# Optimization experiments

Hardware: AMD Instinct MI355X
Metric: run time of the kernel (lower is better)

The kernel has to match this reference:

```python
import jax, jax.numpy as jnp
import numpy as np
import math

B, H, N, D = 2, 16, 8192, 64
NUM_PROJS = 7
BLOCK = 256   # key block size
SAMPLE = 256  # number of sampled columns


def _gray_perm(n):
    # AngularLSH._unit_hamming_distance_array: Gray-code ordering of 2**n buckets
    a = np.array([0, 1], dtype=np.int32)
    for i in range(1, n):
        a = np.concatenate([a, a[::-1] + 2 ** i])
    return a

PERM = jnp.asarray(_gray_perm(NUM_PROJS))
ENC = jnp.asarray(2 ** np.arange(NUM_PROJS), dtype=jnp.int32)


def lsh_hash(x, proj_dir):
    # sign-bit angular LSH, then Gray-code remap so nearby buckets share bits
    bits = (jnp.einsum('bhnd,dr->bhnr', x, proj_dir) > 0).astype(jnp.int32)
    bin_ids = (bits * ENC).sum(-1)
    return PERM[bin_ids]


def take_seq(x, idx):
    # gather along the sequence axis (axis=2); idx is [B,H,M]
    return jnp.take_along_axis(x, idx[..., None], axis=2)


def setup_inputs() -> dict:
    key = jax.random.key(0)
    ks = jax.random.split(key, 5)
    return {
        'query': jax.random.normal(ks[0], (B, H, N, D), jnp.float32),
        'key': jax.random.normal(ks[1], (B, H, N, D), jnp.float32),
        'value': jax.random.normal(ks[2], (B, H, N, D), jnp.float32),
        'proj_dir': jax.random.normal(ks[3], (D + 1, NUM_PROJS), jnp.float32),
        'sampled_set': jax.random.randint(ks[4], (B, H, SAMPLE), 0, N),
    }


def reference(query, key, value, proj_dir, sampled_set):
    scale = D ** -0.5

    # asymmetric MIPS transform: key gets sqrt(max||k||^2 - ||k||^2), query gets 0
    k_norm = jnp.linalg.norm(key, axis=-1)                 # [B,H,N]
    k_max = jnp.max(k_norm, axis=-1, keepdims=True)        # [B,H,1]
    k_extra = jnp.sqrt(jnp.maximum(k_max ** 2 - k_norm ** 2, 0.0))
    key_aug = jnp.concatenate([key, k_extra[..., None]], axis=-1)
    query_aug = jnp.concatenate([query, jnp.zeros_like(query[..., :1])], axis=-1)

    # stable sort by LSH bucket; inverse permutation to un-sort queries at the end
    q_idx = jnp.argsort(lsh_hash(query_aug, proj_dir), axis=2, stable=True)
    k_idx = jnp.argsort(lsh_hash(key_aug, proj_dir), axis=2, stable=True)
    q_idx_inv = jnp.argsort(q_idx, axis=2, stable=True)

    q_s = take_seq(query, q_idx)
    k_s = take_seq(key, k_idx)
    v_s = take_seq(value, k_idx)

    nb = N // BLOCK      # number of key blocks (N divisible by BLOCK here)
    qbs = N // nb        # query block size

    # 1) block-diagonal exact attention over LSH-sorted blocks
    qb = q_s.reshape(B, H, nb, qbs, D)
    kb = k_s.reshape(B, H, nb, BLOCK, D)
    vb = v_s.reshape(B, H, nb, BLOCK, D)
    s_blk = jnp.einsum('bhgqd,bhgkd->bhgqk', qb, kb) * scale
    lse_blk = jax.nn.logsumexp(s_blk, axis=-1)             # [B,H,nb,qbs]
    attn_blk = jnp.einsum('bhgqk,bhgkd->bhgqd', jax.nn.softmax(s_blk, axis=-1), vb)
    attn_blk = attn_blk.reshape(B, H, N, D)
    lse_blk = lse_blk.reshape(B, H, N, 1)

    # 2) residual via uniformly sampled columns; mask out columns already in the
    #    query's own diagonal block to avoid double counting
    k_sub = take_seq(k_s, sampled_set)                     # [B,H,S,D]
    v_sub = take_seq(v_s, sampled_set)
    q_blk_id = jnp.arange(N) // qbs                        # [N]
    covered = q_blk_id[None, None, :, None] == (sampled_set // BLOCK)[:, :, None, :]
    bias = jnp.where(covered, jnp.finfo(q_s.dtype).min, 0.0)
    s_res = jnp.einsum('bhnd,bhsd->bhns', q_s, k_sub) * scale + bias
    # importance weight n_key/sample_size applied in log-space (approximate_unsampled)
    lse_res = jax.nn.logsumexp(s_res, axis=-1, keepdims=True) + math.log(N / SAMPLE)
    attn_res = jnp.einsum('bhns,bhsd->bhnd', jax.nn.softmax(s_res, axis=-1), v_sub)

    # add_self_attentions: merge the two softmax estimates in log-space
    c = 1.0 / (1.0 + jnp.exp(lse_res - lse_blk))
    attn = c * attn_blk + (1.0 - c) * attn_res

    # un-sort rows back to the original query order
    attn = take_seq(attn, q_idx_inv)
    return attn
```

## Files before the change

kernel.cpp:

```cpp
#include <hip/hip_runtime.h>
#include <hip/hip_bf16.h>
#include <math.h>

#define BD 2
#define HD 16
#define NSEQ 8192
#define DDIM 64
#define NPROJ 7
#define KBLK 256
#define NSAMP 256
#define NBH (BD*HD)
#define NB (NSEQ/KBLK)

typedef short bf16x8 __attribute__((ext_vector_type(8)));
typedef short bf16x4 __attribute__((ext_vector_type(4)));
typedef float f32x4 __attribute__((ext_vector_type(4)));

__device__ __forceinline__ unsigned int pk2bf(float a, float b) {
    union { __hip_bfloat162 h; unsigned int u; } t;
    t.h = __float22bfloat162_rn(make_float2(a, b));
    return t.u;
}

__global__ __launch_bounds__(256) void prelude_kernel(const float* __restrict__ q,
                                                      const float* __restrict__ k,
                                                      const float* __restrict__ pd,
                                                      float* __restrict__ kdots,
                                                      unsigned int* __restrict__ kmax_bits,
                                                      unsigned char* __restrict__ qh) {
    __shared__ float pds[(DDIM+1)*NPROJ];
    __shared__ float red[256];
    const int tid = threadIdx.x;
    for (int i = tid; i < (DDIM+1)*NPROJ; i += 256) pds[i] = pd[i];
    __syncthreads();

    const int lin = blockIdx.x * 256 + tid;
    const int bh = lin >> 13;

    float acc[NPROJ];
    float4 xv[16];

    {
        const float4* xp = (const float4*)(q + (size_t)lin * DDIM);
        #pragma unroll
        for (int j = 0; j < 16; ++j) xv[j] = xp[j];
        #pragma unroll
        for (int r = 0; r < NPROJ; ++r) acc[r] = 0.f;
        #pragma unroll
        for (int j = 0; j < 16; ++j) {
            float xs[4] = {xv[j].x, xv[j].y, xv[j].z, xv[j].w};
            #pragma unroll
            for (int c = 0; c < 4; ++c) {
                const int d = j*4 + c;
                #pragma unroll
                for (int r = 0; r < NPROJ; ++r) acc[r] += xs[c] * pds[d*NPROJ + r];
            }
        }
        int bin = 0;
        #pragma unroll
        for (int r = 0; r < NPROJ; ++r) bin |= (acc[r] > 0.f) << r;
        qh[lin] = (unsigned char)(bin ^ (bin >> 1));
    }

    float nr;
    {
        const float4* xp = (const float4*)(k + (size_t)lin * DDIM);
        #pragma unroll
        for (int j = 0; j < 16; ++j) xv[j] = xp[j];
        #pragma unroll
        for (int r = 0; r < NPROJ; ++r) acc[r] = 0.f;
        #pragma unroll
        for (int j = 0; j < 16; ++j) {
            float xs[4] = {xv[j].x, xv[j].y, xv[j].z, xv[j].w};
            #pragma unroll
            for (int c = 0; c < 4; ++c) {
                const int d = j*4 + c;
                #pragma unroll
                for (int r = 0; r < NPROJ; ++r) acc[r] += xs[c] * pds[d*NPROJ + r];
            }
        }
        float ss = 0.f;
        #pragma unroll
        for (int j = 0; j < 16; ++j) {
            float4 t = xv[j];
            ss += t.x*t.x + t.y*t.y + t.z*t.z + t.w*t.w;
        }
        nr = sqrtf(ss);
        float4* kd = (float4*)(kdots + (size_t)lin * 8);
        kd[0] = make_float4(acc[0], acc[1], acc[2], acc[3]);
        kd[1] = make_float4(acc[4], acc[5], acc[6], nr);
    }

    red[tid] = nr;
    __syncthreads();
    for (int s = 128; s > 0; s >>= 1) {
        if (tid < s) red[tid] = fmaxf(red[tid], red[tid+s]);
        __syncthreads();
    }
    if (tid == 0) atomicMax(&kmax_bits[bh], __float_as_uint(red[0]));
}

__global__ __launch_bounds__(256) void khash_kernel(const float* __restrict__ pd,
                                                    const float* __restrict__ kdots,
                                                    const unsigned int* __restrict__ kmax_bits,
                                                    unsigned char* __restrict__ kh) {
    const int lin = blockIdx.x * 256 + threadIdx.x;
    const int bh = lin >> 13;
    const float4* kd = (const float4*)(kdots + (size_t)lin * 8);
    float4 d0 = kd[0], d1 = kd[1];
    float acc[NPROJ] = {d0.x, d0.y, d0.z, d0.w, d1.x, d1.y, d1.z};
    const float kn = d1.w;
    const float km = __uint_as_float(kmax_bits[bh]);
    const float ex = sqrtf(fmaxf(km*km - kn*kn, 0.f));
    int bin = 0;
    #pragma unroll
    for (int r = 0; r < NPROJ; ++r) {
        acc[r] += ex * pd[DDIM*NPROJ + r];
        bin |= (acc[r] > 0.f) << r;
    }
    kh[lin] = (unsigned char)(bin ^ (bin >> 1));
}

__global__ __launch_bounds__(256) void sort_kernel(const unsigned char* __restrict__ qhash,
                                                   const unsigned char* __restrict__ khash,
                                                   int* __restrict__ qidx,
                                                   int* __restrict__ kidx) {
    __shared__ unsigned char hsh[NSEQ];
    __shared__ unsigned short cnt[128][264];
    __shared__ int base[128];
    __shared__ int wtot[2];
    const int bh = blockIdx.x, tid = threadIdx.x;
    const unsigned char* hash = blockIdx.y ? khash : qhash;
    int* idx = blockIdx.y ? kidx : qidx;

    {
        const uint4* src = (const uint4*)(hash + (size_t)bh * NSEQ);
        uint4* hdst = (uint4*)hsh;
        hdst[tid] = src[tid];
        hdst[tid + 256] = src[tid + 256];
        unsigned int* cz = (unsigned int*)&cnt[0][0];
        for (int i = tid; i < 128*264/2; i += 256) cz[i] = 0;
    }
    __syncthreads();
    {
        const unsigned char* s = hsh + tid*32;
        for (int i = 0; i < 32; ++i) cnt[s[i]][tid]++;
    }
    __syncthreads();

    int sc = 0, vv = 0;
    if (tid < 128) {
        unsigned run = 0;
        uint4* rp = (uint4*)cnt[tid];
        for (int wd = 0; wd < 32; ++wd) {
            uint4 x = rp[wd];
            unsigned v0 = x.x & 0xffffu, v1 = x.x >> 16;
            unsigned v2 = x.y & 0xffffu, v3 = x.y >> 16;
            unsigned v4 = x.z & 0xffffu, v5 = x.z >> 16;
            unsigned v6 = x.w & 0xffffu, v7 = x.w >> 16;
            unsigned p0 = run, p1 = p0+v0, p2 = p1+v1, p3 = p2+v2,
                     p4 = p3+v3, p5 = p4+v4, p6 = p5+v5, p7 = p6+v6;
            run = p7 + v7;
            x.x = p0 | (p1<<16); x.y = p2 | (p3<<16);
            x.z = p4 | (p5<<16); x.w = p6 | (p7<<16);
            rp[wd] = x;
        }
        vv = (int)run;
        sc = vv;
        #pragma unroll
        for (int d = 1; d < 64; d <<= 1) {
            int t = __shfl_up(sc, d, 64);
            if ((tid & 63) >= d) sc += t;
        }
        if ((tid & 63) == 63) wtot[tid >> 6] = sc;
    }
    __syncthreads();
    if (tid < 128) base[tid] = (sc - vv) + (tid >= 64 ? wtot[0] : 0);
    __syncthreads();
    {
        int* dst = idx + (size_t)bh * NSEQ;
        const unsigned char* s = hsh + tid*32;
        for (int i = 0; i < 32; ++i) {
            int h = s[i];
            int c = cnt[h][tid];
            cnt[h][tid] = (unsigned short)(c + 1);
            dst[base[h] + c] = tid*32 + i;
        }
    }
}

#define VSWZ(d) ((((d) >> 1) & 7) << 4)

__global__ __launch_bounds__(256) void respack_kernel(const float* __restrict__ k,
                                                      const float* __restrict__ v,
                                                      const int* __restrict__ samp,
                                                      const int* __restrict__ kidx,
                                                      char* __restrict__ kres,
                                                      char* __restrict__ vres) {
    const int bh = blockIdx.x, ch = blockIdx.y, tid = threadIdx.x;
    const size_t basef = (size_t)bh * NSEQ * DDIM;
    char* kimg = kres + (size_t)(bh*4 + ch) * 8192;
    char* vimg = vres + (size_t)(bh*4 + ch) * 8192;

    {
        const int kk = tid & 63, dc = tid >> 6;
        const int sp = samp[bh*NSAMP + ch*64 + kk];
        const int row = kidx[bh*NSEQ + sp];
        const float* kr = k + basef + (size_t)row*DDIM + dc*16;
        float4 f0 = ((const float4*)kr)[0], f1 = ((const float4*)kr)[1];
        float4 f2 = ((const float4*)kr)[2], f3 = ((const float4*)kr)[3];
        union { bf16x8 v8; unsigned int u[4]; } h0, h1;
        h0.u[0] = pk2bf(f0.x,f0.y); h0.u[1] = pk2bf(f0.z,f0.w);
        h0.u[2] = pk2bf(f1.x,f1.y); h0.u[3] = pk2bf(f1.z,f1.w);
        h1.u[0] = pk2bf(f2.x,f2.y); h1.u[1] = pk2bf(f2.z,f2.w);
        h1.u[2] = pk2bf(f3.x,f3.y); h1.u[3] = pk2bf(f3.z,f3.w);
        const int rb = kk*128 + dc*32, sw = (kk & 7) << 4;
        *(bf16x8*)(kimg + ((rb) ^ sw)) = h0.v8;
        *(bf16x8*)(kimg + ((rb + 16) ^ sw)) = h1.v8;
    }
    {
        const int vg = tid & 15, kq = tid >> 4;
        const int r0 = kidx[bh*NSEQ + samp[bh*NSAMP + ch*64 + kq*4 + 0]];
        const int r1 = kidx[bh*NSEQ + samp[bh*NSAMP + ch*64 + kq*4 + 1]];
        const int r2 = kidx[bh*NSEQ + samp[bh*NSAMP + ch*64 + kq*4 + 2]];
        const int r3 = kidx[bh*NSEQ + samp[bh*NSAMP + ch*64 + kq*4 + 3]];
        float4 x0 = *(const float4*)(v + basef + (size_t)r0*DDIM + vg*4);
        float4 x1 = *(const float4*)(v + basef + (size_t)r1*DDIM + vg*4);
        float4 x2 = *(const float4*)(v + basef + (size_t)r2*DDIM + vg*4);
        float4 x3 = *(const float4*)(v + basef + (size_t)r3*DDIM + vg*4);
        const float c0[4] = {x0.x, x0.y, x0.z, x0.w};
        const float c1[4] = {x1.x, x1.y, x1.z, x1.w};
        const float c2[4] = {x2.x, x2.y, x2.z, x2.w};
        const float c3[4] = {x3.x, x3.y, x3.z, x3.w};
        #pragma unroll
        for (int j = 0; j < 4; ++j) {
            const int d = vg*4 + j;
            unsigned h01 = pk2bf(c0[j], c1[j]);
            unsigned h23 = pk2bf(c2[j], c3[j]);
            *(uint2*)(vimg + ((d*128 + kq*8) ^ VSWZ(d))) = make_uint2(h01, h23);
        }
    }
}


#define LN32 3.46573590279972f

template<int PHASE>
__device__ __forceinline__ void compute_chunk(
    int ch, int lane,
    const bf16x8 (&qhf)[4][2], const bf16x8 (&qlf)[4][2],
    f32x4 (&O)[4][4], float (&lacc)[4],
    const float* maskF, const char* KhL, const char* VthL) {

    const int lr4 = lane >> 4;
    const int lc  = lane & 15;

    #pragma unroll
    for (int mt = 0; mt < 4; ++mt) {
        const int key = mt*16 + lc;
        const int ksw = (key & 7) << 4;
        bf16x8 ka0 = *(const bf16x8*)(KhL + ((key*128 +  0 + lr4*16) ^ ksw));
        bf16x8 ka1 = *(const bf16x8*)(KhL + ((key*128 + 64 + lr4*16) ^ ksw));
        float4 mk;
        if (PHASE) mk = *(const float4*)(maskF + ch*64 + mt*16 + lr4*4);

        bf16x4 pb[4];
        #pragma unroll
        for (int qt = 0; qt < 4; ++qt) {
            f32x4 c = {0.f, 0.f, 0.f, 0.f};
            c = __builtin_amdgcn_mfma_f32_16x16x32_bf16(ka0, qhf[qt][0], c, 0, 0, 0);
            c = __builtin_amdgcn_mfma_f32_16x16x32_bf16(ka0, qlf[qt][0], c, 0, 0, 0);
            c = __builtin_amdgcn_mfma_f32_16x16x32_bf16(ka1, qhf[qt][1], c, 0, 0, 0);
            c = __builtin_amdgcn_mfma_f32_16x16x32_bf16(ka1, qlf[qt][1], c, 0, 0, 0);
            float e0, e1, e2, e3;
            if (PHASE) {
                e0 = __expf(c[0] + LN32) * mk.x;
                e1 = __expf(c[1] + LN32) * mk.y;
                e2 = __expf(c[2] + LN32) * mk.z;
                e3 = __expf(c[3] + LN32) * mk.w;
            } else {
                e0 = __expf(c[0]); e1 = __expf(c[1]);
                e2 = __expf(c[2]); e3 = __expf(c[3]);
            }
            lacc[qt] += (e0+e1) + (e2+e3);
            union { bf16x4 v4; unsigned int u[2]; } pw;
            pw.u[0] = pk2bf(e0, e1);
            pw.u[1] = pk2bf(e2, e3);
            pb[qt] = pw.v4;
        }

        __builtin_amdgcn_s_setprio(1);
        #pragma unroll
        for (int dt = 0; dt < 4; ++dt) {
            const int d = dt*16 + lc;
            bf16x4 va = *(const bf16x4*)(VthL + ((d*128 + mt*32 + lr4*8) ^ VSWZ(d)));
            #pragma unroll
            for (int qt = 0; qt < 4; ++qt)
                O[qt][dt] = __builtin_amdgcn_mfma_f32_16x16x16bf16_1k(va, pb[qt], O[qt][dt], 0, 0, 0);
        }
        __builtin_amdgcn_s_setprio(0);
    }
}

__global__ __launch_bounds__(256, 2) void attn_kernel(const float* __restrict__ q,
                                                      const float* __restrict__ k,
                                                      const float* __restrict__ v,
                                                      const int* __restrict__ samp,
                                                      const int* __restrict__ qidx,
                                                      const int* __restrict__ kidx,
                                                      const char* __restrict__ kres,
                                                      const char* __restrict__ vres,
                                                      float* __restrict__ out) {
    __shared__ __align__(16) char KB[8192];
    __shared__ __align__(16) char VB[8192];
    __shared__ int qidxL[256];
    __shared__ int kidxL[256];
    __shared__ float maskF[256];

    const int g = blockIdx.x, bh = blockIdx.y;
    const int tid = threadIdx.x;
    const int lane = tid & 63, w = tid >> 6;
    const int lr4 = lane >> 4, lc = lane & 15;
    const size_t basef = (size_t)bh * NSEQ * DDIM;

    qidxL[tid] = qidx[bh*NSEQ + g*KBLK + tid];
    kidxL[tid] = kidx[bh*NSEQ + g*KBLK + tid];
    {
        int sp = samp[bh*NSAMP + tid];
        maskF[tid] = ((sp >> 8) == g) ? 0.f : 1.f;
    }
    __syncthreads();

    bf16x8 qhf[4][2], qlf[4][2];
    #pragma unroll
    for (int qt = 0; qt < 4; ++qt) {
        const int qrow = qidxL[w*64 + qt*16 + lc];
        const float* qp = q + basef + (size_t)qrow*DDIM;
        #pragma unroll
        for (int ks = 0; ks < 2; ++ks) {
            const float* p = qp + ks*32 + lr4*8;
            float4 a = *(const float4*)p;
            float4 b = *(const float4*)(p + 4);
            float xs[8] = {a.x,a.y,a.z,a.w,b.x,b.y,b.z,b.w};
            union { bf16x8 v8; unsigned int u[4]; } hv, lv;
            #pragma unroll
            for (int j = 0; j < 4; ++j) {
                float s0 = xs[2*j]   * 0.125f;
                float s1 = xs[2*j+1] * 0.125f;
                unsigned hp = pk2bf(s0, s1);
                hv.u[j] = hp;
                float l0 = s0 - __uint_as_float(hp << 16);
                float l1 = s1 - __uint_as_float(hp & 0xffff0000u);
                lv.u[j] = pk2bf(l0, l1);
            }
            qhf[qt][ks] = hv.v8; qlf[qt][ks] = lv.v8;
        }
    }

    f32x4 O[4][4];
    #pragma unroll
    for (int a = 0; a < 4; ++a)
        #pragma unroll
        for (int b = 0; b < 4; ++b) O[a][b] = (f32x4){0.f,0.f,0.f,0.f};
    float lacc[4] = {0,0,0,0};

    const int kk = tid & 63, dcw = tid >> 6;
    const int vg = tid & 15, kq = tid >> 4;

    for (int ch = 0; ch < 4; ++ch) {
        __syncthreads();
        {
            const int korig = kidxL[ch*64 + kk];
            const float* kr = k + basef + (size_t)korig*DDIM + dcw*16;
            float4 f0 = ((const float4*)kr)[0], f1 = ((const float4*)kr)[1];
            float4 f2 = ((const float4*)kr)[2], f3 = ((const float4*)kr)[3];
            union { bf16x8 v8; unsigned int u[4]; } h0, h1;
            h0.u[0] = pk2bf(f0.x,f0.y); h0.u[1] = pk2bf(f0.z,f0.w);
            h0.u[2] = pk2bf(f1.x,f1.y); h0.u[3] = pk2bf(f1.z,f1.w);
            h1.u[0] = pk2bf(f2.x,f2.y); h1.u[1] = pk2bf(f2.z,f2.w);
            h1.u[2] = pk2bf(f3.x,f3.y); h1.u[3] = pk2bf(f3.z,f3.w);
            const int rb = kk*128 + dcw*32, sw2 = (kk & 7) << 4;
            *(bf16x8*)(KB + ((rb) ^ sw2)) = h0.v8;
            *(bf16x8*)(KB + ((rb + 16) ^ sw2)) = h1.v8;
        }
        {
            const int r0 = kidxL[ch*64 + kq*4 + 0];
            const int r1 = kidxL[ch*64 + kq*4 + 1];
            const int r2 = kidxL[ch*64 + kq*4 + 2];
            const int r3 = kidxL[ch*64 + kq*4 + 3];
            float4 x0 = *(const float4*)(v + basef + (size_t)r0*DDIM + vg*4);
            float4 x1 = *(const float4*)(v + basef + (size_t)r1*DDIM + vg*4);
            float4 x2 = *(const float4*)(v + basef + (size_t)r2*DDIM + vg*4);
            float4 x3 = *(const float4*)(v + basef + (size_t)r3*DDIM + vg*4);
            const float c0[4] = {x0.x, x0.y, x0.z, x0.w};
            const float c1[4] = {x1.x, x1.y, x1.z, x1.w};
            const float c2[4] = {x2.x, x2.y, x2.z, x2.w};
            const float c3[4] = {x3.x, x3.y, x3.z, x3.w};
            #pragma unroll
            for (int j = 0; j < 4; ++j) {
                const int d = vg*4 + j;
                unsigned h01 = pk2bf(c0[j], c1[j]);
                unsigned h23 = pk2bf(c2[j], c3[j]);
                *(uint2*)(VB + ((d*128 + kq*8) ^ VSWZ(d))) = make_uint2(h01, h23);
            }
        }
        __syncthreads();
        compute_chunk<0>(ch, lane, qhf, qlf, O, lacc, maskF, KB, VB);
    }

    for (int ch = 0; ch < 4; ++ch) {
        __syncthreads();
        {
            const char* ksrc = kres + (size_t)(bh*4 + ch) * 8192 + tid*32;
            const char* vsrc = vres + (size_t)(bh*4 + ch) * 8192 + tid*32;
            float4 a0 = ((const float4*)ksrc)[0];
            float4 a1 = ((const float4*)ksrc)[1];
            float4 b0 = ((const float4*)vsrc)[0];
            float4 b1 = ((const float4*)vsrc)[1];
            *(float4*)(KB + tid*32)      = a0;
            *(float4*)(KB + tid*32 + 16) = a1;
            *(float4*)(VB + tid*32)      = b0;
            *(float4*)(VB + tid*32 + 16) = b1;
        }
        __syncthreads();
        compute_chunk<1>(ch, lane, qhf, qlf, O, lacc, maskF, KB, VB);
    }

    #pragma unroll
    for (int qt = 0; qt < 4; ++qt) {
        lacc[qt] += __shfl_xor(lacc[qt], 16, 64);
        lacc[qt] += __shfl_xor(lacc[qt], 32, 64);
        lacc[qt] = 1.f / lacc[qt];
    }
    float* ob = out + basef;
    #pragma unroll
    for (int qt = 0; qt < 4; ++qt) {
        const int orow = qidxL[w*64 + qt*16 + lc];
        const float f = lacc[qt];
        float* p = ob + (size_t)orow*DDIM + lr4*4;
        #pragma unroll
        for (int dt = 0; dt < 4; ++dt) {
            float4 st = make_float4(O[qt][dt][0]*f, O[qt][dt][1]*f,
                                    O[qt][dt][2]*f, O[qt][dt][3]*f);
            *(float4*)(p + dt*16) = st;
        }
    }
}

extern "C" void kernel_launch(void* const* d_in, const int* in_sizes, int n_in,
                              void* d_out, int out_size, void* d_ws, size_t ws_size,
                              hipStream_t stream) {
    const float* q    = (const float*)d_in[0];
    const float* k    = (const float*)d_in[1];
    const float* v    = (const float*)d_in[2];
    const float* pd   = (const float*)d_in[3];
    const int*   samp = (const int*)d_in[4];
    float* out = (float*)d_out;

    char* ws = (char*)d_ws;
    float*         kdots = (float*)(ws + 0);
    int*           qidx  = (int*)(ws + 0);
    int*           kidx  = (int*)(ws + 1048576);
    char*          kres  = ws + 2097152;
    char*          vres  = ws + 3145728;
    unsigned char* qh    = (unsigned char*)(ws + 8388608);
    unsigned char* kh    = (unsigned char*)(ws + 8650752);
    unsigned int*  kmaxb = (unsigned int*)(ws + 8912896);

    hipMemsetAsync(kmaxb, 0, NBH*sizeof(unsigned int), stream);
    hipLaunchKernelGGL(prelude_kernel, dim3(NBH*NSEQ/256), dim3(256), 0, stream,
                       q, k, pd, kdots, kmaxb, qh);
    hipLaunchKernelGGL(khash_kernel, dim3(NBH*NSEQ/256), dim3(256), 0, stream,
                       pd, kdots, kmaxb, kh);
    hipLaunchKernelGGL(sort_kernel, dim3(NBH, 2), dim3(256), 0, stream, qh, kh, qidx, kidx);
    hipLaunchKernelGGL(respack_kernel, dim3(NBH, 4), dim3(256), 0, stream,
                       k, v, samp, kidx, kres, vres);
    hipLaunchKernelGGL(attn_kernel, dim3(NB, NBH), dim3(256), 0, stream,
                       q, k, v, samp, qidx, kidx, kres, vres, out);
}
```

Measured before the change: 157.5 us.

## Stage two key chunks per barrier and prefetch next chunk via global_load_lds

```diff
diff --git a/kernel.cpp b/kernel.cpp
--- a/kernel.cpp
+++ b/kernel.cpp
@@ -20,6 +20,12 @@
     union { __hip_bfloat162 h; unsigned int u; } t;
     t.h = __float22bfloat162_rn(make_float2(a, b));
     return t.u;
+}
+
+__device__ __forceinline__ void gload16(const void* gsrc, void* lds) {
+    __builtin_amdgcn_global_load_lds(
+        (const __attribute__((address_space(1))) unsigned int*)gsrc,
+        (__attribute__((address_space(3))) unsigned int*)lds, 16, 0, 0);
 }
 
 __global__ __launch_bounds__(256) void prelude_kernel(const float* __restrict__ q,
@@ -197,16 +203,17 @@
                                                       const int* __restrict__ kidx,
                                                       char* __restrict__ kres,
                                                       char* __restrict__ vres) {
+    __shared__ int rows[64];
     const int bh = blockIdx.x, ch = blockIdx.y, tid = threadIdx.x;
+    if (tid < 64) rows[tid] = kidx[bh*NSEQ + samp[bh*NSAMP + ch*64 + tid]];
+    __syncthreads();
     const size_t basef = (size_t)bh * NSEQ * DDIM;
     char* kimg = kres + (size_t)(bh*4 + ch) * 8192;
     char* vimg = vres + (size_t)(bh*4 + ch) * 8192;
 
     {
         const int kk = tid & 63, dc = tid >> 6;
-        const int sp = samp[bh*NSAMP + ch*64 + kk];
-        const int row = kidx[bh*NSEQ + sp];
-        const float* kr = k + basef + (size_t)row*DDIM + dc*16;
+        const float* kr = k + basef + (size_t)rows[kk]*DDIM + dc*16;
         float4 f0 = ((const float4*)kr)[0], f1 = ((const float4*)kr)[1];
         float4 f2 = ((const float4*)kr)[2], f3 = ((const float4*)kr)[3];
         union { bf16x8 v8; unsigned int u[4]; } h0, h1;
@@ -220,10 +227,8 @@
     }
     {
         const int vg = tid & 15, kq = tid >> 4;
-        const int r0 = kidx[bh*NSEQ + samp[bh*NSAMP + ch*64 + kq*4 + 0]];
-        const int r1 = kidx[bh*NSEQ + samp[bh*NSAMP + ch*64 + kq*4 + 1]];
-        const int r2 = kidx[bh*NSEQ + samp[bh*NSAMP + ch*64 + kq*4 + 2]];
-        const int r3 = kidx[bh*NSEQ + samp[bh*NSAMP + ch*64 + kq*4 + 3]];
+        const int r0 = rows[kq*4 + 0], r1 = rows[kq*4 + 1];
+        const int r2 = rows[kq*4 + 2], r3 = rows[kq*4 + 3];
         float4 x0 = *(const float4*)(v + basef + (size_t)r0*DDIM + vg*4);
         float4 x1 = *(const float4*)(v + basef + (size_t)r1*DDIM + vg*4);
         float4 x2 = *(const float4*)(v + basef + (size_t)r2*DDIM + vg*4);
@@ -311,11 +316,12 @@
                                                       const char* __restrict__ kres,
                                                       const char* __restrict__ vres,
                                                       float* __restrict__ out) {
-    __shared__ __align__(16) char KB[8192];
-    __shared__ __align__(16) char VB[8192];
+    __shared__ __align__(16) char KB[2][8192];
+    __shared__ __align__(16) char VB[2][8192];
     __shared__ int qidxL[256];
     __shared__ int kidxL[256];
-    __shared__ float maskF[256];
+    __shared__ __align__(16) float maskF[256];
+    __shared__ __align__(16) char PFD[1024];
 
     const int g = blockIdx.x, bh = blockIdx.y;
     const int tid = threadIdx.x;
@@ -364,66 +370,86 @@
         for (int b = 0; b < 4; ++b) O[a][b] = (f32x4){0.f,0.f,0.f,0.f};
     float lacc[4] = {0,0,0,0};
 
-    const int kk = tid & 63, dcw = tid >> 6;
-    const int vg = tid & 15, kq = tid >> 4;
-
-    for (int ch = 0; ch < 4; ++ch) {
+    const int kk2 = tid & 127, cck = kk2 >> 6, kkr = kk2 & 63, dc2 = tid >> 7;
+    const int vg = tid & 15, m2 = tid >> 4;
+    const int ccv = m2 >> 3, kqb = (m2 & 7) * 2;
+
+    for (int st = 0; st < 2; ++st) {
         __syncthreads();
         {
-            const int korig = kidxL[ch*64 + kk];
-            const float* kr = k + basef + (size_t)korig*DDIM + dcw*16;
-            float4 f0 = ((const float4*)kr)[0], f1 = ((const float4*)kr)[1];
-            float4 f2 = ((const float4*)kr)[2], f3 = ((const float4*)kr)[3];
-            union { bf16x8 v8; unsigned int u[4]; } h0, h1;
-            h0.u[0] = pk2bf(f0.x,f0.y); h0.u[1] = pk2bf(f0.z,f0.w);
-            h0.u[2] = pk2bf(f1.x,f1.y); h0.u[3] = pk2bf(f1.z,f1.w);
-            h1.u[0] = pk2bf(f2.x,f2.y); h1.u[1] = pk2bf(f2.z,f2.w);
-            h1.u[2] = pk2bf(f3.x,f3.y); h1.u[3] = pk2bf(f3.z,f3.w);
-            const int rb = kk*128 + dcw*32, sw2 = (kk & 7) << 4;
-            *(bf16x8*)(KB + ((rb) ^ sw2)) = h0.v8;
-            *(bf16x8*)(KB + ((rb + 16) ^ sw2)) = h1.v8;
+            const int row = kidxL[st*128 + kk2];
+            const float* kr = k + basef + (size_t)row*DDIM + dc2*32;
+            float4 f[8];
+            #pragma unroll
+            for (int i = 0; i < 8; ++i) f[i] = ((const float4*)kr)[i];
+            const int sw2 = (kkr & 7) << 4;
+            #pragma unroll
+            for (int gi = 0; gi < 4; ++gi) {
+                union { bf16x8 v8; unsigned int u[4]; } h;
+                h.u[0] = pk2bf(f[2*gi].x,   f[2*gi].y);
+                h.u[1] = pk2bf(f[2*gi].z,   f[2*gi].w);
+                h.u[2] = pk2bf(f[2*gi+1].x, f[2*gi+1].y);
+                h.u[3] = pk2bf(f[2*gi+1].z, f[2*gi+1].w);
+                *(bf16x8*)(KB[cck] + ((kkr*128 + dc2*64 + gi*16) ^ sw2)) = h.v8;
+            }
         }
         {
-            const int r0 = kidxL[ch*64 + kq*4 + 0];
-            const int r1 = kidxL[ch*64 + kq*4 + 1];
-            const int r2 = kidxL[ch*64 + kq*4 + 2];
-            const int r3 = kidxL[ch*64 + kq*4 + 3];
-            float4 x0 = *(const float4*)(v + basef + (size_t)r0*DDIM + vg*4);
-            float4 x1 = *(const float4*)(v + basef + (size_t)r1*DDIM + vg*4);
-            float4 x2 = *(const float4*)(v + basef + (size_t)r2*DDIM + vg*4);
-            float4 x3 = *(const float4*)(v + basef + (size_t)r3*DDIM + vg*4);
-            const float c0[4] = {x0.x, x0.y, x0.z, x0.w};
-            const float c1[4] = {x1.x, x1.y, x1.z, x1.w};
-            const float c2[4] = {x2.x, x2.y, x2.z, x2.w};
-            const float c3[4] = {x3.x, x3.y, x3.z, x3.w};
-            #pragma unroll
-            for (int j = 0; j < 4; ++j) {
-                const int d = vg*4 + j;
-                unsigned h01 = pk2bf(c0[j], c1[j]);
-                unsigned h23 = pk2bf(c2[j], c3[j]);
-                *(uint2*)(VB + ((d*128 + kq*8) ^ VSWZ(d))) = make_uint2(h01, h23);
+            float4 x[8];
+            #pragma unroll
+            for (int i = 0; i < 8; ++i) {
+                const int r = kidxL[st*128 + m2*8 + i];
+                x[i] = *(const float4*)(v + basef + (size_t)r*DDIM + vg*4);
+            }
+            #pragma unroll
+            for (int kqq = 0; kqq < 2; ++kqq) {
+                const float c0[4] = {x[kqq*4+0].x, x[kqq*4+0].y, x[kqq*4+0].z, x[kqq*4+0].w};
+                const float c1[4] = {x[kqq*4+1].x, x[kqq*4+1].y, x[kqq*4+1].z, x[kqq*4+1].w};
+                const float c2[4] = {x[kqq*4+2].x, x[kqq*4+2].y, x[kqq*4+2].z, x[kqq*4+2].w};
+                const float c3[4] = {x[kqq*4+3].x, x[kqq*4+3].y, x[kqq*4+3].z, x[kqq*4+3].w};
+                #pragma unroll
+                for (int j = 0; j < 4; ++j) {
+                    const int d = vg*4 + j;
+                    unsigned h01 = pk2bf(c0[j], c1[j]);
+                    unsigned h23 = pk2bf(c2[j], c3[j]);
+                    *(uint2*)(VB[ccv] + ((d*128 + (kqb + kqq)*8) ^ VSWZ(d))) = make_uint2(h01, h23);
+                }
             }
         }
         __syncthreads();
-        compute_chunk<0>(ch, lane, qhf, qlf, O, lacc, maskF, KB, VB);
-    }
-
-    for (int ch = 0; ch < 4; ++ch) {
+
+        if (st == 0) {
+            const int prow = kidxL[128 + (tid & 127)];
+            const char* kb = (const char*)(k + basef) + (size_t)prow*256 + (tid >> 7)*128;
+            const char* vb = (const char*)(v + basef) + (size_t)prow*256 + (tid >> 7)*128;
+            gload16(kb, PFD);
+            gload16(vb, PFD);
+        } else {
+            gload16(kres + (size_t)bh*32768 + tid*128, PFD);
+            gload16(vres + (size_t)bh*32768 + tid*128, PFD);
+        }
+
+        compute_chunk<0>(st*2 + 0, lane, qhf, qlf, O, lacc, maskF, KB[0], VB[0]);
+        compute_chunk<0>(st*2 + 1, lane, qhf, qlf, O, lacc, maskF, KB[1], VB[1]);
+    }
+
+    for (int st = 0; st < 2; ++st) {
         __syncthreads();
-        {
-            const char* ksrc = kres + (size_t)(bh*4 + ch) * 8192 + tid*32;
-            const char* vsrc = vres + (size_t)(bh*4 + ch) * 8192 + tid*32;
+        #pragma unroll
+        for (int cc = 0; cc < 2; ++cc) {
+            const char* ksrc = kres + (size_t)(bh*4 + st*2 + cc) * 8192 + tid*32;
+            const char* vsrc = vres + (size_t)(bh*4 + st*2 + cc) * 8192 + tid*32;
             float4 a0 = ((const float4*)ksrc)[0];
             float4 a1 = ((const float4*)ksrc)[1];
             float4 b0 = ((const float4*)vsrc)[0];
             float4 b1 = ((const float4*)vsrc)[1];
-            *(float4*)(KB + tid*32)      = a0;
-            *(float4*)(KB + tid*32 + 16) = a1;
-            *(float4*)(VB + tid*32)      = b0;
-            *(float4*)(VB + tid*32 + 16) = b1;
+            *(float4*)(KB[cc] + tid*32)      = a0;
+            *(float4*)(KB[cc] + tid*32 + 16) = a1;
+            *(float4*)(VB[cc] + tid*32)      = b0;
+            *(float4*)(VB[cc] + tid*32 + 16) = b1;
         }
         __syncthreads();
-        compute_chunk<1>(ch, lane, qhf, qlf, O, lacc, maskF, KB, VB);
+        compute_chunk<1>(st*2 + 0, lane, qhf, qlf, O, lacc, maskF, KB[0], VB[0]);
+        compute_chunk<1>(st*2 + 1, lane, qhf, qlf, O, lacc, maskF, KB[1], VB[1]);
     }
 
     #pragma unroll
@@ -440,9 +466,9 @@
         float* p = ob + (size_t)orow*DDIM + lr4*4;
         #pragma unroll
         for (int dt = 0; dt < 4; ++dt) {
-            float4 st = make_float4(O[qt][dt][0]*f, O[qt][dt][1]*f,
-                                    O[qt][dt][2]*f, O[qt][dt][3]*f);
-            *(float4*)(p + dt*16) = st;
+            float4 st4 = make_float4(O[qt][dt][0]*f, O[qt][dt][1]*f,
+                                     O[qt][dt][2]*f, O[qt][dt][3]*f);
+            *(float4*)(p + dt*16) = st4;
         }
     }
 }
```

Measured after the change: 317.6 us. 102% more time.
